# Optimization experiments

Measured on AMD Instinct MI355X. Metric: run time of the kernel, lower is better.

## Reference

```python
import jax, jax.numpy as jnp
import numpy as np

HEADS = 16
D_MODEL = 1024
D_K = D_MODEL // HEADS


def setup_inputs() -> dict:
    key = jax.random.key(0)
    ks = jax.random.split(key, 8)
    B, S = 4, 2048
    scale = 1.0 / np.sqrt(D_MODEL)
    return {
        "queries": jax.random.normal(ks[0], (B, S, D_MODEL), dtype=jnp.float32),
        "keys": jax.random.normal(ks[1], (B, S, D_MODEL), dtype=jnp.float32),
        "values": jax.random.normal(ks[2], (B, S, D_MODEL), dtype=jnp.float32),
        # Per-head projection weights, stacked over heads: [H, d_model, d_k]
        "Wq": jax.random.normal(ks[3], (HEADS, D_MODEL, D_K), dtype=jnp.float32) * scale,
        "Wk": jax.random.normal(ks[4], (HEADS, D_MODEL, D_K), dtype=jnp.float32) * scale,
        "Wv": jax.random.normal(ks[5], (HEADS, D_MODEL, D_K), dtype=jnp.float32) * scale,
        "Wout": jax.random.normal(ks[6], (D_MODEL, D_MODEL), dtype=jnp.float32) * scale,
        "bout": jax.random.normal(ks[7], (D_MODEL,), dtype=jnp.float32) * 0.01,
    }


def reference(queries, keys, values, Wq, Wk, Wv, Wout, bout):
    # Per-head linear projections (torch Linear: x @ W.T, here W stored as [H, d_model, d_k])
    q = jnp.einsum("bsd,hdk->bhsk", queries, Wq)   # [B,H,S,d_k]
    k = jnp.einsum("btd,hdk->bhtk", keys, Wk)      # [B,H,T,d_k]
    v = jnp.einsum("btd,hdv->bhtv", values, Wv)    # [B,H,T,d_v]
    scores = jnp.einsum("bhsk,bhtk->bhst", q, k) / jnp.sqrt(jnp.float32(D_K))
    probs = jax.nn.softmax(scores, axis=-1)        # [B,H,S,T]
    wv = jnp.einsum("bhst,bhtv->bhsv", probs, v)   # [B,H,S,d_v]
    # concat heads along last dim: [B,S,H*d_v] == [B,S,d_model]
    B, H, S, Dv = wv.shape
    concat = jnp.transpose(wv, (0, 2, 1, 3)).reshape(B, S, H * Dv)
    return concat @ Wout.T + bout
```

## Files before the change

kernel.cpp:

```cpp
#include <hip/hip_runtime.h>
#include <hip/hip_bf16.h>
#include <stdint.h>

#define DM 1024
#define SZ ((size_t)8192*1024)
#define WSZ ((size_t)1024*1024)

typedef float  f32x4  __attribute__((ext_vector_type(4)));
typedef float  f32x16 __attribute__((ext_vector_type(16)));
typedef __bf16 bf16x8 __attribute__((ext_vector_type(8)));
typedef __bf16 bf16x2 __attribute__((ext_vector_type(2)));
typedef short  s16x8  __attribute__((ext_vector_type(8)));
typedef unsigned int u32;
typedef unsigned int u32x4 __attribute__((ext_vector_type(4)));

typedef const __attribute__((address_space(1))) void* gas_ptr;
typedef __attribute__((address_space(3))) void* las_ptr;

static __device__ __forceinline__ f32x4 mfma16(s16x8 a, s16x8 b, f32x4 c){
  return __builtin_amdgcn_mfma_f32_16x16x32_bf16(
      __builtin_bit_cast(bf16x8, a), __builtin_bit_cast(bf16x8, b), c, 0, 0, 0);
}
static __device__ __forceinline__ f32x16 mfma32(s16x8 a, s16x8 b, f32x16 c){
  return __builtin_amdgcn_mfma_f32_32x32x16_bf16(
      __builtin_bit_cast(bf16x8, a), __builtin_bit_cast(bf16x8, b), c, 0, 0, 0);
}

static __device__ __forceinline__ u32 pack2(float a, float b){
  bf16x2 v = { (__bf16)a, (__bf16)b };
  return __builtin_bit_cast(u32, v);
}
static __device__ __forceinline__ short f2bf(float f){
  __bf16 v = (__bf16)f;
  return __builtin_bit_cast(short, v);
}

static __device__ __forceinline__ void gload_lds16(void* l, const void* g){
  __builtin_amdgcn_global_load_lds((gas_ptr)g, (las_ptr)l, 16, 0, 0);
}

#define QSCALE 0.1803368801111444f


__global__ void convert_misc(const float* __restrict__ q, const float* __restrict__ k,
                             const float* __restrict__ v, const float* __restrict__ wo,
                             short* __restrict__ ws){
  const size_t n8_in  = (3*SZ)/8;
  const size_t n8_tot = n8_in + WSZ/8;
  size_t stride = (size_t)gridDim.x * blockDim.x;
  for (size_t c = (size_t)blockIdx.x*blockDim.x + threadIdx.x; c < n8_tot; c += stride){
    const float* src; short* dst;
    if (c < n8_in){
      size_t e = c*8;
      int s = (int)(e / SZ);
      size_t off = e - (size_t)s*SZ;
      src = (s==0 ? q : (s==1 ? k : v)) + off;
      dst = ws + e;
    } else {
      size_t off = (c - n8_in)*8;
      src = wo + off;
      dst = ws + 6*SZ + 3*WSZ + off;
    }
    float4 a = *(const float4*)src;
    float4 b = *(const float4*)(src + 4);
    uint4 o;
    o.x = pack2(a.x, a.y); o.y = pack2(a.z, a.w);
    o.z = pack2(b.x, b.y); o.w = pack2(b.z, b.w);
    *(uint4*)dst = o;
  }
}

__global__ void convert_wqkv(const float* __restrict__ wq, const float* __restrict__ wk,
                             const float* __restrict__ wv, short* __restrict__ ws){
  __shared__ float tile[64][65];
  int bid = blockIdx.x;
  int sel = bid >> 8;
  int h   = (bid >> 4) & 15;
  int dt  = bid & 15;
  const float* W = sel==0 ? wq : (sel==1 ? wk : wv);
  float sc = sel==0 ? QSCALE : 1.0f;
  short* Bt = ws + 6*SZ + (size_t)sel*WSZ;
  int tid = threadIdx.x;
  int r = tid >> 4, c4 = (tid & 15)*4;
  int d0 = dt*64;
  #pragma unroll
  for (int i=0;i<4;i++){
    int d = r + i*16;
    float4 vv = *(const float4*)&W[(size_t)h*65536 + (size_t)(d0+d)*64 + c4];
    tile[d][c4+0]=vv.x*sc; tile[d][c4+1]=vv.y*sc; tile[d][c4+2]=vv.z*sc; tile[d][c4+3]=vv.w*sc;
  }
  __syncthreads();
  #pragma unroll
  for (int i=0;i<4;i++){
    int kk = r + i*16;
    unsigned int lo = pack2(tile[c4+0][kk], tile[c4+1][kk]);
    unsigned int hi = pack2(tile[c4+2][kk], tile[c4+3][kk]);
    *(uint2*)&Bt[(size_t)(h*64+kk)*1024 + d0 + c4] = make_uint2(lo, hi);
  }
}


static __device__ __forceinline__ void gemm_core(
    const short* __restrict__ A, const short* __restrict__ Bt,
    int bm, int bn, short* As, short* Bs, f32x4 acc[4][4])
{
  int tid = threadIdx.x;
  int w = tid>>6, lane = tid&63;
  int wm = w>>1, wn = w&1;
  int col = lane&15, kg = lane>>4;
  int rs = w*16 + (lane>>2);
  int ch = lane&3;

  auto stage = [&](int buf, int kt){
    #pragma unroll
    for (int it=0; it<2; ++it){
      int r = rs + it*64;
      gload_lds16(As + buf*4096 + r*32 + ch*8,
                  A + (size_t)(bm*128 + r)*1024 + kt*32 + ch*8);
    }
    #pragma unroll
    for (int it=0; it<2; ++it){
      int r = rs + it*64;
      gload_lds16(Bs + buf*4096 + r*32 + ch*8,
                  Bt + (size_t)(bn*128 + r)*1024 + kt*32 + ch*8);
    }
  };

  const f32x4 fzero = {0.f,0.f,0.f,0.f};
  #pragma unroll
  for (int mf=0; mf<4; ++mf)
    #pragma unroll
    for (int nf=0; nf<4; ++nf)
      acc[mf][nf] = fzero;

  stage(0, 0);
  int buf = 0;
  for (int kt=0; kt<32; ++kt){
    __syncthreads();
    if (kt < 31) stage(buf^1, kt+1);
    s16x8 af[4], bfr[4];
    #pragma unroll
    for (int mf=0; mf<4; ++mf)
      af[mf] = *(const s16x8*)(As + buf*4096 + (wm*64 + mf*16 + col)*32 + kg*8);
    #pragma unroll
    for (int nf=0; nf<4; ++nf)
      bfr[nf] = *(const s16x8*)(Bs + buf*4096 + (wn*64 + nf*16 + col)*32 + kg*8);
    #pragma unroll
    for (int mf=0; mf<4; ++mf)
      #pragma unroll
      for (int nf=0; nf<4; ++nf)
        acc[mf][nf] = mfma16(af[mf], bfr[nf], acc[mf][nf]);
    buf ^= 1;
  }
}

__global__ __launch_bounds__(256,2) void gemm_qkv(short* __restrict__ ws){
  __shared__ __align__(16) short As[2*4096];
  __shared__ __align__(16) short Bs[2*4096];
  int bid = blockIdx.x;
  bid = (bid & 7)*192 + (bid >> 3);
  int bm = bid / 24, bnq = bid % 24;
  int sel = bnq >> 3, bn = bnq & 7;
  const short* A  = ws + (size_t)sel*SZ;
  const short* Bt = ws + 6*SZ + (size_t)sel*WSZ;
  f32x4 acc[4][4];
  gemm_core(A, Bt, bm, bn, As, Bs, acc);

  int tid = threadIdx.x, w = tid>>6, lane = tid&63;
  int wm=w>>1, wn=w&1, col=lane&15, kg=lane>>4;
  if (sel < 2){
    short* O = ws + (size_t)(3+sel)*SZ;
    #pragma unroll
    for (int mf=0; mf<4; ++mf){
      int gr0 = bm*128 + wm*64 + mf*16 + kg*4;
      #pragma unroll
      for (int nf=0; nf<4; ++nf){
        int gc = bn*128 + wn*64 + nf*16 + col;
        #pragma unroll
        for (int r=0; r<4; ++r)
          O[(size_t)(gr0+r)*1024 + gc] = f2bf(acc[mf][nf][r]);
      }
    }
  } else {
    short* V = ws + 5*SZ;
    #pragma unroll
    for (int mf=0; mf<4; ++mf){
      int gr0 = bm*128 + wm*64 + mf*16 + kg*4;
      int b = gr0 >> 11, s0 = gr0 & 2047;
      #pragma unroll
      for (int nf=0; nf<4; ++nf){
        int gc = bn*128 + wn*64 + nf*16 + col;
        int h = gc >> 6, dv = gc & 63;
        unsigned int lo = pack2(acc[mf][nf][0], acc[mf][nf][1]);
        unsigned int hi = pack2(acc[mf][nf][2], acc[mf][nf][3]);
        *(uint2*)&V[((size_t)((b*16+h)*64+dv))*2048 + s0] = make_uint2(lo, hi);
      }
    }
  }
}

__global__ __launch_bounds__(256,2) void gemm_out(const short* __restrict__ cc,
                                                  const short* __restrict__ BtO,
                                                  const float* __restrict__ bias,
                                                  float* __restrict__ out){
  __shared__ __align__(16) short As[2*4096];
  __shared__ __align__(16) short Bs[2*4096];
  int bid = blockIdx.x;
  bid = (bid & 7)*64 + (bid >> 3);
  int bm = bid >> 3, bn = bid & 7;
  f32x4 acc[4][4];
  gemm_core(cc, BtO, bm, bn, As, Bs, acc);

  int tid = threadIdx.x, w=tid>>6, lane=tid&63;
  int wm=w>>1, wn=w&1, col=lane&15, kg=lane>>4;
  #pragma unroll
  for (int nf=0; nf<4; ++nf){
    int gc = bn*128 + wn*64 + nf*16 + col;
    float bb = bias[gc];
    #pragma unroll
    for (int mf=0; mf<4; ++mf){
      int gr0 = bm*128 + wm*64 + mf*16 + kg*4;
      #pragma unroll
      for (int r=0; r<4; ++r)
        out[(size_t)(gr0+r)*1024 + gc] = acc[mf][nf][r] + bb;
    }
  }
}

__global__ __launch_bounds__(256,3) void attn(const short* __restrict__ qp,
                                              const short* __restrict__ kp,
                                              const short* __restrict__ vT,
                                              short* __restrict__ cc){
  __shared__ __align__(16) short Ks[2][4096];
  __shared__ __align__(16) short Vs[2][4096];
  int bid = blockIdx.x;
  bid = (bid & 7)*128 + (bid >> 3);
  int qt = bid & 15, h = (bid>>4) & 15, b = bid >> 8;
  int tid = threadIdx.x, w = tid>>6, lane = tid&63;
  int ql = lane & 31, hi = lane >> 5;
  int qrow = qt*128 + w*32 + ql;

  const short* qg = qp + ((size_t)(b*2048 + qrow))*1024 + h*64;
  s16x8 qf[4];
  #pragma unroll
  for (int ks=0; ks<4; ++ks)
    qf[ks] = *(const s16x8*)(qg + ks*16 + hi*8);

  const short* kb = kp + (size_t)(b*2048)*1024 + h*64;
  const short* vb = vT + (size_t)((b*16 + h)*64)*2048;

  int kb0 = ql*128 + ((hi ^ (ql & 7)) << 4);
  int koff[4];
  #pragma unroll
  for (int ks=0; ks<4; ++ks) koff[ks] = kb0 ^ (ks << 5);

  int rl = lane>>3, chc = lane&7;
  int r0 = w*8 + rl, r1 = 32 + w*8 + rl;
  const short* ksrc0 = kb + (size_t)r0*1024 + (chc ^ (r0 & 7))*8;
  const short* ksrc1 = kb + (size_t)r1*1024 + (chc ^ (r1 & 7))*8;
  const short* vsrc0 = vb + (size_t)r0*2048 + (chc ^ (r0 & 7))*8;
  const short* vsrc1 = vb + (size_t)r1*2048 + (chc ^ (r1 & 7))*8;

  auto stage = [&](int buf, int t0){
    gload_lds16(&Ks[buf][r0*64 + chc*8], ksrc0 + (size_t)t0*1024);
    gload_lds16(&Ks[buf][r1*64 + chc*8], ksrc1 + (size_t)t0*1024);
    gload_lds16(&Vs[buf][r0*64 + chc*8], vsrc0 + t0);
    gload_lds16(&Vs[buf][r1*64 + chc*8], vsrc1 + t0);
  };

  const f32x16 z16 = {0.f,0.f,0.f,0.f,0.f,0.f,0.f,0.f,
                      0.f,0.f,0.f,0.f,0.f,0.f,0.f,0.f};
  f32x16 o0 = z16, o1 = z16;
  float l = 0.f;

  auto body = [&](int buf){
    const char* kt = (const char*)Ks + buf*8192;
    const char* vt = (const char*)Vs + buf*8192;
    f32x16 s0 = z16, s1 = z16;
    __builtin_amdgcn_s_setprio(1);
    #pragma unroll
    for (int ks=0; ks<4; ++ks){
      s16x8 k0 = *(const s16x8*)(kt + koff[ks]);
      s16x8 k1 = *(const s16x8*)(kt + 4096 + koff[ks]);
      s0 = mfma32(k0, qf[ks], s0);
      s1 = mfma32(k1, qf[ks], s1);
    }
    __builtin_amdgcn_s_setprio(0);

    float la=0.f, lb=0.f, lc=0.f, ld=0.f;
    #pragma unroll
    for (int i=0;i<16;i+=4){
      s0[i]   = __builtin_amdgcn_exp2f(s0[i]);   la += s0[i];
      s0[i+1] = __builtin_amdgcn_exp2f(s0[i+1]); lb += s0[i+1];
      s0[i+2] = __builtin_amdgcn_exp2f(s0[i+2]); lc += s0[i+2];
      s0[i+3] = __builtin_amdgcn_exp2f(s0[i+3]); ld += s0[i+3];
    }
    #pragma unroll
    for (int i=0;i<16;i+=4){
      s1[i]   = __builtin_amdgcn_exp2f(s1[i]);   la += s1[i];
      s1[i+1] = __builtin_amdgcn_exp2f(s1[i+1]); lb += s1[i+1];
      s1[i+2] = __builtin_amdgcn_exp2f(s1[i+2]); lc += s1[i+2];
      s1[i+3] = __builtin_amdgcn_exp2f(s1[i+3]); ld += s1[i+3];
    }
    l += (la+lb)+(lc+ld);

    s16x8 pb[4];
    {
      u32 a0 = pack2(s0[0], s0[1]),  b0 = pack2(s0[2], s0[3]);
      u32 c0 = pack2(s0[4], s0[5]),  d0 = pack2(s0[6], s0[7]);
      asm("v_permlane32_swap_b32 %0, %1" : "+v"(a0), "+v"(c0));
      asm("v_permlane32_swap_b32 %0, %1" : "+v"(b0), "+v"(d0));
      u32x4 t0v = {a0, b0, c0, d0};
      pb[0] = __builtin_bit_cast(s16x8, t0v);
      u32 a1 = pack2(s0[8], s0[9]),  b1 = pack2(s0[10], s0[11]);
      u32 c1 = pack2(s0[12], s0[13]),d1 = pack2(s0[14], s0[15]);
      asm("v_permlane32_swap_b32 %0, %1" : "+v"(a1), "+v"(c1));
      asm("v_permlane32_swap_b32 %0, %1" : "+v"(b1), "+v"(d1));
      u32x4 t1v = {a1, b1, c1, d1};
      pb[1] = __builtin_bit_cast(s16x8, t1v);
      u32 a2 = pack2(s1[0], s1[1]),  b2 = pack2(s1[2], s1[3]);
      u32 c2 = pack2(s1[4], s1[5]),  d2 = pack2(s1[6], s1[7]);
      asm("v_permlane32_swap_b32 %0, %1" : "+v"(a2), "+v"(c2));
      asm("v_permlane32_swap_b32 %0, %1" : "+v"(b2), "+v"(d2));
      u32x4 t2v = {a2, b2, c2, d2};
      pb[2] = __builtin_bit_cast(s16x8, t2v);
      u32 a3 = pack2(s1[8], s1[9]),  b3 = pack2(s1[10], s1[11]);
      u32 c3 = pack2(s1[12], s1[13]),d3 = pack2(s1[14], s1[15]);
      asm("v_permlane32_swap_b32 %0, %1" : "+v"(a3), "+v"(c3));
      asm("v_permlane32_swap_b32 %0, %1" : "+v"(b3), "+v"(d3));
      u32x4 t3v = {a3, b3, c3, d3};
      pb[3] = __builtin_bit_cast(s16x8, t3v);
    }

    __builtin_amdgcn_s_setprio(1);
    #pragma unroll
    for (int ks2=0; ks2<4; ++ks2){
      s16x8 v0 = *(const s16x8*)(vt + koff[ks2]);
      s16x8 v1 = *(const s16x8*)(vt + 4096 + koff[ks2]);
      o0 = mfma32(v0, pb[ks2], o0);
      o1 = mfma32(v1, pb[ks2], o1);
    }
    __builtin_amdgcn_s_setprio(0);
  };

  stage(0, 0);
  for (int t = 0; t < 32; t += 2){
    __syncthreads();
    stage(1, (t+1)*64);
    body(0);
    __syncthreads();
    if (t+2 < 32) stage(0, (t+2)*64);
    body(1);
  }

  l += __shfl_xor(l, 32);
  float rcl = 1.0f / l;
  short* og = cc + ((size_t)(b*2048 + qrow))*1024 + h*64;
  #pragma unroll
  for (int s=0; s<4; ++s){
    int dv0 = s*8 + hi*4;
    uint2 w0, w1;
    w0.x = pack2(o0[s*4+0]*rcl, o0[s*4+1]*rcl);
    w0.y = pack2(o0[s*4+2]*rcl, o0[s*4+3]*rcl);
    *(uint2*)&og[dv0] = w0;
    w1.x = pack2(o1[s*4+0]*rcl, o1[s*4+1]*rcl);
    w1.y = pack2(o1[s*4+2]*rcl, o1[s*4+3]*rcl);
    *(uint2*)&og[32 + dv0] = w1;
  }
}


extern "C" void kernel_launch(void* const* d_in, const int* in_sizes, int n_in,
                              void* d_out, int out_size, void* d_ws, size_t ws_size,
                              hipStream_t stream){
  const float* q  = (const float*)d_in[0];
  const float* k  = (const float*)d_in[1];
  const float* v  = (const float*)d_in[2];
  const float* wq = (const float*)d_in[3];
  const float* wk = (const float*)d_in[4];
  const float* wv = (const float*)d_in[5];
  const float* wo = (const float*)d_in[6];
  const float* bo = (const float*)d_in[7];
  short* ws = (short*)d_ws;
  float* out = (float*)d_out;

  size_t needed = (6*SZ + 4*WSZ)*sizeof(short);
  if (ws_size < needed) return;

  convert_misc<<<2048, 256, 0, stream>>>(q, k, v, wo, ws);
  convert_wqkv<<<768, 256, 0, stream>>>(wq, wk, wv, ws);
  gemm_qkv<<<1536, 256, 0, stream>>>(ws);
  attn<<<1024, 256, 0, stream>>>(ws + 3*SZ, ws + 4*SZ, ws + 5*SZ, ws);
  gemm_out<<<512, 256, 0, stream>>>(ws, ws + 6*SZ + 3*WSZ, bo, out);
}
```

Measured before the change: 209.4 us.

## Pre-tile K and V in fragment order and double query rows per wave

The QKV GEMM epilogue now writes K and V into a per-head, per-32-key tile layout that matches the MFMA fragment order, so the attention kernel loads them into LDS with contiguous, swizzle-free copies. Each attention wave now handles 64 query rows instead of 32 and reuses each K/V fragment across two query tiles. This halves the grid and LDS traffic per output while using 32-key tiles. The cost is more accumulator registers, occupancy lowered from 3 to 2 blocks, twice as many loop iterations with smaller tiles, and scattered 2-byte stores in the K epilogue.

```diff
diff --git a/kernel.cpp b/kernel.cpp
--- a/kernel.cpp
+++ b/kernel.cpp
@@ -168,8 +168,8 @@
 
   int tid = threadIdx.x, w = tid>>6, lane = tid&63;
   int wm=w>>1, wn=w&1, col=lane&15, kg=lane>>4;
-  if (sel < 2){
-    short* O = ws + (size_t)(3+sel)*SZ;
+  if (sel == 0){
+    short* O = ws + 3*SZ;
     #pragma unroll
     for (int mf=0; mf<4; ++mf){
       int gr0 = bm*128 + wm*64 + mf*16 + kg*4;
@@ -181,19 +181,38 @@
           O[(size_t)(gr0+r)*1024 + gc] = f2bf(acc[mf][nf][r]);
       }
     }
-  } else {
-    short* V = ws + 5*SZ;
+  } else if (sel == 1){
+    short* Kt = ws + 4*SZ;
     #pragma unroll
     for (int mf=0; mf<4; ++mf){
       int gr0 = bm*128 + wm*64 + mf*16 + kg*4;
       int b = gr0 >> 11, s0 = gr0 & 2047;
+      int ts = s0 >> 5, t0 = s0 & 31;
+      #pragma unroll
+      for (int nf=0; nf<4; ++nf){
+        int gc = bn*128 + wn*64 + nf*16 + col;
+        int h = gc >> 6, d = gc & 63;
+        size_t base = ((size_t)((b*16+h)*64 + ts))*2048 + (size_t)((d>>3)*32)*8 + (d&7);
+        #pragma unroll
+        for (int r=0; r<4; ++r)
+          Kt[base + (size_t)(t0+r)*8] = f2bf(acc[mf][nf][r]);
+      }
+    }
+  } else {
+    short* Vt = ws + 5*SZ;
+    #pragma unroll
+    for (int mf=0; mf<4; ++mf){
+      int gr0 = bm*128 + wm*64 + mf*16 + kg*4;
+      int b = gr0 >> 11, s0 = gr0 & 2047;
+      int ts = s0 >> 5, c2 = (s0 >> 3) & 3, j0 = s0 & 7;
       #pragma unroll
       for (int nf=0; nf<4; ++nf){
         int gc = bn*128 + wn*64 + nf*16 + col;
         int h = gc >> 6, dv = gc & 63;
         unsigned int lo = pack2(acc[mf][nf][0], acc[mf][nf][1]);
         unsigned int hi = pack2(acc[mf][nf][2], acc[mf][nf][3]);
-        *(uint2*)&V[((size_t)((b*16+h)*64+dv))*2048 + s0] = make_uint2(lo, hi);
+        size_t addr = ((size_t)((b*16+h)*64 + ts))*2048 + (size_t)(c2*64 + dv)*8 + j0;
+        *(uint2*)&Vt[addr] = make_uint2(lo, hi);
       }
     }
   }
@@ -227,63 +246,73 @@
   }
 }
 
-__global__ __launch_bounds__(256,3) void attn(const short* __restrict__ qp,
-                                              const short* __restrict__ kp,
-                                              const short* __restrict__ vT,
+__global__ __launch_bounds__(256,2) void attn(const short* __restrict__ qp,
+                                              const short* __restrict__ kpT,
+                                              const short* __restrict__ vTt,
                                               short* __restrict__ cc){
-  __shared__ __align__(16) short Ks[2][4096];
-  __shared__ __align__(16) short Vs[2][4096];
+  __shared__ __align__(16) short Ks[2][2048];
+  __shared__ __align__(16) short Vs[2][2048];
   int bid = blockIdx.x;
-  bid = (bid & 7)*128 + (bid >> 3);
-  int qt = bid & 15, h = (bid>>4) & 15, b = bid >> 8;
+  bid = (bid & 7)*64 + (bid >> 3);
+  int qb = bid & 7, h = (bid>>3) & 15, b = bid >> 7;
   int tid = threadIdx.x, w = tid>>6, lane = tid&63;
   int ql = lane & 31, hi = lane >> 5;
-  int qrow = qt*128 + w*32 + ql;
-
-  const short* qg = qp + ((size_t)(b*2048 + qrow))*1024 + h*64;
-  s16x8 qf[4];
-  #pragma unroll
-  for (int ks=0; ks<4; ++ks)
-    qf[ks] = *(const s16x8*)(qg + ks*16 + hi*8);
-
-  const short* kb = kp + (size_t)(b*2048)*1024 + h*64;
-  const short* vb = vT + (size_t)((b*16 + h)*64)*2048;
-
-  int kb0 = ql*128 + ((hi ^ (ql & 7)) << 4);
-  int koff[4];
-  #pragma unroll
-  for (int ks=0; ks<4; ++ks) koff[ks] = kb0 ^ (ks << 5);
-
-  int rl = lane>>3, chc = lane&7;
-  int r0 = w*8 + rl, r1 = 32 + w*8 + rl;
-  const short* ksrc0 = kb + (size_t)r0*1024 + (chc ^ (r0 & 7))*8;
-  const short* ksrc1 = kb + (size_t)r1*1024 + (chc ^ (r1 & 7))*8;
-  const short* vsrc0 = vb + (size_t)r0*2048 + (chc ^ (r0 & 7))*8;
-  const short* vsrc1 = vb + (size_t)r1*2048 + (chc ^ (r1 & 7))*8;
-
-  auto stage = [&](int buf, int t0){
-    gload_lds16(&Ks[buf][r0*64 + chc*8], ksrc0 + (size_t)t0*1024);
-    gload_lds16(&Ks[buf][r1*64 + chc*8], ksrc1 + (size_t)t0*1024);
-    gload_lds16(&Vs[buf][r0*64 + chc*8], vsrc0 + t0);
-    gload_lds16(&Vs[buf][r1*64 + chc*8], vsrc1 + t0);
+  int qbase = qb*256 + w*64;
+
+  const short* qg = qp + ((size_t)(b*2048 + qbase + ql))*1024 + h*64;
+  s16x8 qf[2][4];
+  #pragma unroll
+  for (int qt=0; qt<2; ++qt)
+    #pragma unroll
+    for (int ks=0; ks<4; ++ks)
+      qf[qt][ks] = *(const s16x8*)(qg + qt*32*1024 + ks*16 + hi*8);
+
+  const short* ktb = kpT + ((size_t)((b*16 + h)*64))*2048;
+  const short* vtb = vTt + ((size_t)((b*16 + h)*64))*2048;
+
+  int koff = hi*512 + ql*16;
+  int voff = hi*1024 + ql*16;
+
+  const short* sgb = (w < 2) ? ktb : vtb;
+  short* ldb = (w < 2) ? &Ks[0][0] : &Vs[0][0];
+  int jj = (w & 1) * 1024;
+  auto stage = [&](int buf, int ti){
+    const short* src = sgb + (size_t)ti*2048 + jj + lane*8;
+    short* dst = ldb + buf*2048 + jj + lane*8;
+    gload_lds16(dst, src);
+    gload_lds16(dst + 512, src + 512);
   };
 
   const f32x16 z16 = {0.f,0.f,0.f,0.f,0.f,0.f,0.f,0.f,
                       0.f,0.f,0.f,0.f,0.f,0.f,0.f,0.f};
-  f32x16 o0 = z16, o1 = z16;
-  float l = 0.f;
+  f32x16 o[2][2] = {{z16, z16}, {z16, z16}};
+  float l0 = 0.f, l1 = 0.f;
+
+  auto packP = [&](f32x16& s, s16x8* pb){
+    u32 a0 = pack2(s[0], s[1]),  b0 = pack2(s[2], s[3]);
+    u32 c0 = pack2(s[4], s[5]),  d0 = pack2(s[6], s[7]);
+    asm("v_permlane32_swap_b32 %0, %1" : "+v"(a0), "+v"(c0));
+    asm("v_permlane32_swap_b32 %0, %1" : "+v"(b0), "+v"(d0));
+    u32x4 t0v = {a0, b0, c0, d0};
+    pb[0] = __builtin_bit_cast(s16x8, t0v);
+    u32 a1 = pack2(s[8], s[9]),   b1 = pack2(s[10], s[11]);
+    u32 c1 = pack2(s[12], s[13]), d1 = pack2(s[14], s[15]);
+    asm("v_permlane32_swap_b32 %0, %1" : "+v"(a1), "+v"(c1));
+    asm("v_permlane32_swap_b32 %0, %1" : "+v"(b1), "+v"(d1));
+    u32x4 t1v = {a1, b1, c1, d1};
+    pb[1] = __builtin_bit_cast(s16x8, t1v);
+  };
 
   auto body = [&](int buf){
-    const char* kt = (const char*)Ks + buf*8192;
-    const char* vt = (const char*)Vs + buf*8192;
+    const char* kt = (const char*)Ks + buf*4096;
+    const char* vt = (const char*)Vs + buf*4096;
     f32x16 s0 = z16, s1 = z16;
     __builtin_amdgcn_s_setprio(1);
     #pragma unroll
     for (int ks=0; ks<4; ++ks){
-      s16x8 k0 = *(const s16x8*)(kt + koff[ks]);
-      s16x8 k1 = *(const s16x8*)(kt + 4096 + koff[ks]);
-      s0 = mfma32(k0, qf[ks], s0);
-      s1 = mfma32(k1, qf[ks], s1);
+      s16x8 kf = *(const s16x8*)(kt + koff + ks*1024);
+      s0 = mfma32(kf, qf[0][ks], s0);
+      s1 = mfma32(kf, qf[1][ks], s1);
     }
     __builtin_amdgcn_s_setprio(0);
 
@@ -295,77 +324,62 @@
       s0[i+2] = __builtin_amdgcn_exp2f(s0[i+2]); lc += s0[i+2];
       s0[i+3] = __builtin_amdgcn_exp2f(s0[i+3]); ld += s0[i+3];
     }
+    l0 += (la+lb)+(lc+ld);
+    float le=0.f, lf=0.f, lg=0.f, lh=0.f;
     #pragma unroll
     for (int i=0;i<16;i+=4){
-      s1[i]   = __builtin_amdgcn_exp2f(s1[i]);   la += s1[i];
-      s1[i+1] = __builtin_amdgcn_exp2f(s1[i+1]); lb += s1[i+1];
-      s1[i+2] = __builtin_amdgcn_exp2f(s1[i+2]); lc += s1[i+2];
-      s1[i+3] = __builtin_amdgcn_exp2f(s1[i+3]); ld += s1[i+3];
-    }
-    l += (la+lb)+(lc+ld);
-
-    s16x8 pb[4];
-    {
-      u32 a0 = pack2(s0[0], s0[1]),  b0 = pack2(s0[2], s0[3]);
-      u32 c0 = pack2(s0[4], s0[5]),  d0 = pack2(s0[6], s0[7]);
-      asm("v_permlane32_swap_b32 %0, %1" : "+v"(a0), "+v"(c0));
-      asm("v_permlane32_swap_b32 %0, %1" : "+v"(b0), "+v"(d0));
-      u32x4 t0v = {a0, b0, c0, d0};
-      pb[0] = __builtin_bit_cast(s16x8, t0v);
-      u32 a1 = pack2(s0[8], s0[9]),  b1 = pack2(s0[10], s0[11]);
-      u32 c1 = pack2(s0[12], s0[13]),d1 = pack2(s0[14], s0[15]);
-      asm("v_permlane32_swap_b32 %0, %1" : "+v"(a1), "+v"(c1));
-      asm("v_permlane32_swap_b32 %0, %1" : "+v"(b1), "+v"(d1));
-      u32x4 t1v = {a1, b1, c1, d1};
-      pb[1] = __builtin_bit_cast(s16x8, t1v);
-      u32 a2 = pack2(s1[0], s1[1]),  b2 = pack2(s1[2], s1[3]);
-      u32 c2 = pack2(s1[4], s1[5]),  d2 = pack2(s1[6], s1[7]);
-      asm("v_permlane32_swap_b32 %0, %1" : "+v"(a2), "+v"(c2));
-      asm("v_permlane32_swap_b32 %0, %1" : "+v"(b2), "+v"(d2));
-      u32x4 t2v = {a2, b2, c2, d2};
-      pb[2] = __builtin_bit_cast(s16x8, t2v);
-      u32 a3 = pack2(s1[8], s1[9]),  b3 = pack2(s1[10], s1[11]);
-      u32 c3 = pack2(s1[12], s1[13]),d3 = pack2(s1[14], s1[15]);
-      asm("v_permlane32_swap_b32 %0, %1" : "+v"(a3), "+v"(c3));
-      asm("v_permlane32_swap_b32 %0, %1" : "+v"(b3), "+v"(d3));
-      u32x4 t3v = {a3, b3, c3, d3};
-      pb[3] = __builtin_bit_cast(s16x8, t3v);
-    }
+      s1[i]   = __builtin_amdgcn_exp2f(s1[i]);   le += s1[i];
+      s1[i+1] = __builtin_amdgcn_exp2f(s1[i+1]); lf += s1[i+1];
+      s1[i+2] = __builtin_amdgcn_exp2f(s1[i+2]); lg += s1[i+2];
+      s1[i+3] = __builtin_amdgcn_exp2f(s1[i+3]); lh += s1[i+3];
+    }
+    l1 += (le+lf)+(lg+lh);
+
+    s16x8 pb0[2], pb1[2];
+    packP(s0, pb0);
+    packP(s1, pb1);
 
     __builtin_amdgcn_s_setprio(1);
     #pragma unroll
-    for (int ks2=0; ks2<4; ++ks2){
-      s16x8 v0 = *(const s16x8*)(vt + koff[ks2]);
-      s16x8 v1 = *(const s16x8*)(vt + 4096 + koff[ks2]);
-      o0 = mfma32(v0, pb[ks2], o0);
-      o1 = mfma32(v1, pb[ks2], o1);
+    for (int ks2=0; ks2<2; ++ks2){
+      #pragma unroll
+      for (int dvt=0; dvt<2; ++dvt){
+        s16x8 vf = *(const s16x8*)(vt + voff + ks2*2048 + dvt*512);
+        o[0][dvt] = mfma32(vf, pb0[ks2], o[0][dvt]);
+        o[1][dvt] = mfma32(vf, pb1[ks2], o[1][dvt]);
+      }
     }
     __builtin_amdgcn_s_setprio(0);
   };
 
   stage(0, 0);
-  for (int t = 0; t < 32; t += 2){
+  for (int ti = 0; ti < 64; ti += 2){
     __syncthreads();
-    stage(1, (t+1)*64);
+    stage(1, ti+1);
     body(0);
     __syncthreads();
-    if (t+2 < 32) stage(0, (t+2)*64);
+    if (ti+2 < 64) stage(0, ti+2);
     body(1);
   }
 
-  l += __shfl_xor(l, 32);
-  float rcl = 1.0f / l;
-  short* og = cc + ((size_t)(b*2048 + qrow))*1024 + h*64;
-  #pragma unroll
-  for (int s=0; s<4; ++s){
-    int dv0 = s*8 + hi*4;
-    uint2 w0, w1;
-    w0.x = pack2(o0[s*4+0]*rcl, o0[s*4+1]*rcl);
-    w0.y = pack2(o0[s*4+2]*rcl, o0[s*4+3]*rcl);
-    *(uint2*)&og[dv0] = w0;
-    w1.x = pack2(o1[s*4+0]*rcl, o1[s*4+1]*rcl);
-    w1.y = pack2(o1[s*4+2]*rcl, o1[s*4+3]*rcl);
-    *(uint2*)&og[32 + dv0] = w1;
+  l0 += __shfl_xor(l0, 32);
+  l1 += __shfl_xor(l1, 32);
+  float rc0 = 1.0f / l0, rc1 = 1.0f / l1;
+  #pragma unroll
+  for (int qt=0; qt<2; ++qt){
+    float rcl = qt ? rc1 : rc0;
+    short* og = cc + ((size_t)(b*2048 + qbase + qt*32 + ql))*1024 + h*64;
+    #pragma unroll
+    for (int dvt=0; dvt<2; ++dvt){
+      #pragma unroll
+      for (int s=0; s<4; ++s){
+        int dv0 = dvt*32 + s*8 + hi*4;
+        uint2 wd;
+        wd.x = pack2(o[qt][dvt][s*4+0]*rcl, o[qt][dvt][s*4+1]*rcl);
+        wd.y = pack2(o[qt][dvt][s*4+2]*rcl, o[qt][dvt][s*4+3]*rcl);
+        *(uint2*)&og[dv0] = wd;
+      }
+    }
   }
 }
 
@@ -390,6 +404,6 @@
   convert_misc<<<2048, 256, 0, stream>>>(q, k, v, wo, ws);
   convert_wqkv<<<768, 256, 0, stream>>>(wq, wk, wv, ws);
   gemm_qkv<<<1536, 256, 0, stream>>>(ws);
-  attn<<<1024, 256, 0, stream>>>(ws + 3*SZ, ws + 4*SZ, ws + 5*SZ, ws);
+  attn<<<512, 256, 0, stream>>>(ws + 3*SZ, ws + 4*SZ, ws + 5*SZ, ws);
   gemm_out<<<512, 256, 0, stream>>>(ws, ws + 6*SZ + 3*WSZ, bo, out);
 }
```

New measurement: 201.4 us. -3.8%, faster.
